# Performance work log

Measured on AMD Instinct MI355X. Metric: run time of the kernel, lower is better.

Reference implementation:

```python
import jax, jax.numpy as jnp
import numpy as np

L, N, M = 128, 512, 256   # batch-like dim, recurrence length, feature dim (M_size1)
TK, H = 4, 8              # num_blocks, num_heads
DH = M // H
EPS = 1e-5


def setup_inputs() -> dict:
    key = jax.random.key(0)
    ks = jax.random.split(key, 8)
    s = 0.05  # scale raw-randn params for numerical stability
    return {
        "x": jax.random.normal(ks[0], (L, N, M), jnp.float32),
        "weight": jax.random.normal(ks[1], (M, M), jnp.float32) * s,
        "Wqkv": jax.random.normal(ks[2], (TK, 3, H, DH, M), jnp.float32) * s,
        "Wo": jax.random.normal(ks[3], (TK, M, M), jnp.float32) * s,
        "ln_g": jnp.ones((M,), jnp.float32),
        "ln_b": jnp.zeros((M,), jnp.float32),
        "lnz_g": jnp.ones((M,), jnp.float32),
        "lnz_b": jnp.zeros((M,), jnp.float32),
        "fc1_w": jax.random.normal(ks[4], (4 * M, M), jnp.float32) / np.float32(np.sqrt(M)),
        "fc1_b": jnp.zeros((4 * M,), jnp.float32),
        "fc2_w": jax.random.normal(ks[5], (M, 4 * M), jnp.float32) / np.float32(np.sqrt(4 * M)),
        "fc2_b": jnp.zeros((M,), jnp.float32),
    }


def _ln(x, g, b):
    mu = x.mean(-1, keepdims=True)
    var = x.var(-1, keepdims=True)  # biased variance, as torch LayerNorm
    return (x - mu) * jax.lax.rsqrt(var + EPS) * g + b


def _pos_bias(dtype):
    # bias[j, z]   = sin(j / 10000**(2z/M)) for even z
    # bias[j, z+1] = cos(j / 10000**(2z/M))
    pos = jnp.arange(N, dtype=dtype)                      # j
    z = jnp.arange(0, M, 2, dtype=dtype)                  # even indices
    ang = pos[:, None] / (10000.0 ** (2.0 * z / M))       # (N, M/2)
    return jnp.stack([jnp.sin(ang), jnp.cos(ang)], axis=-1).reshape(N, M)


def reference(x, weight, Wqkv, Wo, ln_g, ln_b, lnz_g, lnz_b, fc1_w, fc1_b, fc2_w, fc2_b):
    # savespace: (L, N, M); positional bias depends only on (j, feature)
    s = jnp.einsum('lm,ijm->ijl', weight, x) + _pos_bias(x.dtype)[None]
    inv_sqrt_dh = np.float32(1.0 / np.sqrt(DH))
    for a in range(TK):
        qkv = jnp.einsum('xhdm,ijm->xijhd', Wqkv[a], _ln(s, ln_g, ln_b))
        q, k, v = qkv[0], qkv[1], qkv[2]                  # each (L, N, H, DH)
        rsa = jnp.einsum('ijhd,ijhd->ijh', q * inv_sqrt_dh, k)
        imv = rsa[..., None] * v                           # (L, N, H, DH)
        imv = jnp.cumsum(imv, axis=1)                      # retention recurrence over j
        s = jnp.einsum('nm,ijm->ijn', Wo[a], imv.reshape(L, N, M)) + s
        s = _ln(s, lnz_g, lnz_b) + s
        h = jax.nn.gelu(s @ fc1_w.T + fc1_b, approximate=False)
        s = h @ fc2_w.T + fc2_b
    return s
```

## Files before the change

### kernel.cpp

```cpp
#include <hip/hip_runtime.h>

typedef unsigned int u32;
typedef unsigned short u16;
typedef _Float16 f16;
typedef __attribute__((ext_vector_type(8))) _Float16 f16x8;
typedef __attribute__((ext_vector_type(4))) float f32x4;
typedef __attribute__((ext_vector_type(4))) u16 u16x4;

#define L_ 128
#define N_ 512
#define M_ 256
#define TK_ 4
#define H_ 8
#define R_ (L_*N_)
#define FF_ 1024

__device__ __forceinline__ u16 f2h(float v){ f16 h=(f16)v; return __builtin_bit_cast(u16,h); }
__device__ __forceinline__ float h2f(u16 b){ return (float)__builtin_bit_cast(f16,b); }
__device__ __forceinline__ f32x4 mfmah(f16x8 a, f16x8 b, f32x4 c){
  return __builtin_amdgcn_mfma_f32_16x16x32_f16(a,b,c,0,0,0);
}
__device__ __forceinline__ float gelu_f(float x){
  float u = x*(0.7978845608f + 0.0356774081f*x*x);
  float e = __expf(u + u);
  float r = __builtin_amdgcn_rcpf(e + 1.f);
  return x - x*r;
}


__global__ void k_bias(float* __restrict__ bias){
  int j = blockIdx.x, l = threadIdx.x;
  int t = l>>1;
  float base = expf(-0.14391156831212757f * (float)t);
  float ang = (float)j * base;
  bias[j*M_ + l] = (l&1) ? cosf(ang) : sinf(ang);
}

__global__ void k_pack(const float* __restrict__ src, u16* __restrict__ dst, int K){
  int b = blockIdx.x; int nk = K>>6; int cg = b/nk, k64 = b%nk;
  int t = threadIdx.x;
  int st = t>>6, g = (t>>4)&3, lr = t&15;
  const float* sp = src + (cg*16+lr)*K + k64*64 + st*32 + g*8;
  f16x8 hv;
  #pragma unroll
  for (int e=0;e<8;e++) hv[e] = (f16)sp[e];
  *(f16x8*)(dst + b*1024 + t*8) = hv;
}

__global__ void k_pack_qkv(const float* __restrict__ w, u16* __restrict__ dst){
  int b = blockIdx.x;
  int a = b/192; int rmn = b%192; int grp = rmn>>2, k64 = rmn&3;
  int hd = grp/6, cidx = grp%6;
  int t = threadIdx.x;
  int st = t>>6, g = (t>>4)&3, lr = t&15;
  int cl = cidx*16 + lr;
  int x = cl>>5, d = cl&31;
  const float* sp = w + (((a*3+x)*H_+hd)*32 + d)*M_ + k64*64 + st*32 + g*8;
  f16x8 hv;
  #pragma unroll
  for (int e=0;e<8;e++) hv[e] = (f16)sp[e];
  *(f16x8*)(dst + b*1024 + t*8) = hv;
}

__device__ __forceinline__ void stageA16(const u16* __restrict__ src, u16* __restrict__ Abuf,
                                         int rowbase, int tid){
  int row = tid>>3, skh = tid&7;
  int k64 = skh>>1, st = skh&1;
  int rg = row>>4, lr = row&15;
  const u16* sp = src + (rowbase+row)*M_ + k64*64 + st*32;
  u16* dp = Abuf + (k64*4+rg)*1024 + st*512 + lr*8;
  #pragma unroll
  for (int gg=0;gg<4;gg++)
    *(uint4*)(dp + gg*128) = *(const uint4*)(sp + gg*8);
}

__global__ __launch_bounds__(512) void k_init(const float* __restrict__ X, const u16* __restrict__ Wf,
    const float* __restrict__ bias, const float* __restrict__ lg, const float* __restrict__ lb,
    float* __restrict__ out, u16* __restrict__ P1){
  __shared__ __align__(16) u16 Abuf[16*1024];
  __shared__ float zs[8][64][2];
  int tid = threadIdx.x;
  int wx = tid>>6, lane = tid&63;
  int g = lane>>4, lr = lane&15;
  int lo = g*128 + lr*8;
  int rowbase = blockIdx.x*64;
  {
    int row = tid>>3, skh = tid&7;
    int k64 = skh>>1, st = skh&1;
    int rg = row>>4, slr = row&15;
    const float* sp = X + (rowbase+row)*M_ + k64*64 + st*32;
    u16* dp = Abuf + (k64*4+rg)*1024 + st*512 + slr*8;
    #pragma unroll
    for (int gg=0;gg<4;gg++){
      f16x8 hv;
      #pragma unroll
      for (int e=0;e<8;e++) hv[e] = (f16)sp[gg*8+e];
      *(f16x8*)(dp + gg*128) = hv;
    }
  }
  __syncthreads();
  f32x4 acc[4][2];
  #pragma unroll
  for (int i=0;i<4;i++){ acc[i][0]=0.f; acc[i][1]=0.f; }
  #pragma unroll
  for (int k64=0;k64<4;k64++)
    #pragma unroll
    for (int st=0;st<2;st++){
      f16x8 a[4], b[2];
      #pragma unroll
      for (int i=0;i<4;i++) a[i] = *(const f16x8*)(Abuf + (k64*4 + i)*1024 + st*512 + lo);
      #pragma unroll
      for (int j=0;j<2;j++) b[j] = *(const f16x8*)(Wf + ((wx*2+j)*4 + k64)*1024 + st*512 + lo);
      #pragma unroll
      for (int i=0;i<4;i++)
        #pragma unroll
        for (int j=0;j<2;j++) acc[i][j] = mfmah(a[i], b[j], acc[i][j]);
    }
  #pragma unroll
  for (int i=0;i<4;i++)
    #pragma unroll
    for (int j=0;j<2;j++)
      #pragma unroll
      for (int r=0;r<4;r++){
        int row = rowbase + i*16 + g*4 + r;
        int col = wx*32 + j*16 + lr;
        acc[i][j][r] += bias[(row & (N_-1))*M_ + col];
        out[row*M_ + col] = acc[i][j][r];
      }
  #pragma unroll
  for (int i=0;i<4;i++)
    #pragma unroll
    for (int r=0;r<4;r++){
      float ps = 0.f, qs = 0.f;
      #pragma unroll
      for (int j=0;j<2;j++){ float t = acc[i][j][r]; ps += t; qs += t*t; }
      ps += __shfl_xor(ps,1); qs += __shfl_xor(qs,1);
      ps += __shfl_xor(ps,2); qs += __shfl_xor(qs,2);
      ps += __shfl_xor(ps,4); qs += __shfl_xor(qs,4);
      ps += __shfl_xor(ps,8); qs += __shfl_xor(qs,8);
      if (lr == 0){
        int rowl = i*16 + g*4 + r;
        zs[wx][rowl][0] = ps;
        zs[wx][rowl][1] = qs;
      }
    }
  __syncthreads();
  #pragma unroll
  for (int i=0;i<4;i++)
    #pragma unroll
    for (int r=0;r<4;r++){
      int rowl = i*16 + g*4 + r;
      float sum=0.f, sq=0.f;
      #pragma unroll
      for (int q=0;q<8;q++){ sum += zs[q][rowl][0]; sq += zs[q][rowl][1]; }
      float mean = sum*(1.f/M_);
      float var  = sq*(1.f/M_) - mean*mean;
      float rstd = rsqrtf(var + 1e-5f);
      int row = rowbase + rowl;
      #pragma unroll
      for (int j=0;j<2;j++){
        int col = wx*32 + j*16 + lr;
        P1[row*M_ + col] = f2h((acc[i][j][r]-mean)*rstd*lg[col] + lb[col]);
      }
    }
}

__global__ __launch_bounds__(512) void k_qkv(const u16* __restrict__ P1, const u16* __restrict__ Wq,
    u16* __restrict__ imv){
  __shared__ __align__(16) u16 Abuf[16*1024];
  int tid = threadIdx.x;
  int hd = tid>>6, lane = tid&63;
  int g = lane>>4, lr = lane&15;
  int lo = g*128 + lr*8;
  int rowbase = blockIdx.x*64;
  stageA16(P1, Abuf, rowbase, tid);
  __syncthreads();
  f32x4 acc[4][6];
  #pragma unroll
  for (int i=0;i<4;i++)
    #pragma unroll
    for (int c=0;c<6;c++) acc[i][c] = 0.f;
  const u16* Wb = Wq + hd*6*4096;
  #pragma unroll
  for (int k64=0;k64<4;k64++)
    #pragma unroll
    for (int st=0;st<2;st++){
      f16x8 a[4];
      #pragma unroll
      for (int i=0;i<4;i++) a[i] = *(const f16x8*)(Abuf + (k64*4 + i)*1024 + st*512 + lo);
      #pragma unroll
      for (int c=0;c<6;c++){
        f16x8 b = *(const f16x8*)(Wb + (c*4 + k64)*1024 + st*512 + lo);
        #pragma unroll
        for (int i=0;i<4;i++) acc[i][c] = mfmah(a[i], b, acc[i][c]);
      }
    }
  const float isd = 0.17677669529663687f;
  #pragma unroll
  for (int i=0;i<4;i++){
    f32x4 p = acc[i][0]*acc[i][2] + acc[i][1]*acc[i][3];
    #pragma unroll
    for (int r=0;r<4;r++){
      float v = p[r];
      v += __shfl_xor(v,1); v += __shfl_xor(v,2);
      v += __shfl_xor(v,4); v += __shfl_xor(v,8);
      float rsa = v * isd;
      int row = rowbase + i*16 + g*4 + r;
      imv[row*M_ + hd*32 + lr]      = f2h(rsa*acc[i][4][r]);
      imv[row*M_ + hd*32 + 16 + lr] = f2h(rsa*acc[i][5][r]);
    }
  }
}

__global__ __launch_bounds__(256) void k_scan(const u16* __restrict__ imv, u16* __restrict__ P1){
  __shared__ float tot[4][64];
  int bi = blockIdx.x;
  int i = bi>>2, mc = bi&3;
  int tid = threadIdx.x;
  int ml = tid&63, jc = tid>>6;
  int m = mc*64 + ml;
  int base = i*N_*M_ + jc*128*M_ + m;
  float acc = 0.f;
  for (int jb=0;jb<128;jb+=8){
    float t[8];
    #pragma unroll
    for (int u=0;u<8;u++) t[u] = h2f(imv[base + (jb+u)*M_]);
    #pragma unroll
    for (int u=0;u<8;u++) acc += t[u];
  }
  tot[jc][ml] = acc;
  __syncthreads();
  float pre = 0.f;
  #pragma unroll
  for (int q=0;q<3;q++) if (q<jc) pre += tot[q][ml];
  acc = pre;
  for (int jb=0;jb<128;jb+=8){
    float t[8];
    #pragma unroll
    for (int u=0;u<8;u++) t[u] = h2f(imv[base + (jb+u)*M_]);
    #pragma unroll
    for (int u=0;u<8;u++){ acc += t[u]; P1[base + (jb+u)*M_] = f2h(acc); }
  }
}

__global__ __launch_bounds__(512) void k_wo(u16* __restrict__ P1, const u16* __restrict__ Wf,
    const float* __restrict__ sold, const float* __restrict__ lg, const float* __restrict__ lb){
  __shared__ __align__(16) u16 Abuf[16*1024];
  __shared__ float zs[8][64][2];
  int tid = threadIdx.x;
  int wx = tid>>6, lane = tid&63;
  int g = lane>>4, lr = lane&15;
  int lo = g*128 + lr*8;
  int rowbase = blockIdx.x*64;
  stageA16(P1, Abuf, rowbase, tid);
  __syncthreads();
  f32x4 acc[4][2];
  #pragma unroll
  for (int i=0;i<4;i++){ acc[i][0]=0.f; acc[i][1]=0.f; }
  #pragma unroll
  for (int k64=0;k64<4;k64++)
    #pragma unroll
    for (int st=0;st<2;st++){
      f16x8 a[4], b[2];
      #pragma unroll
      for (int i=0;i<4;i++) a[i] = *(const f16x8*)(Abuf + (k64*4 + i)*1024 + st*512 + lo);
      #pragma unroll
      for (int j=0;j<2;j++) b[j] = *(const f16x8*)(Wf + ((wx*2+j)*4 + k64)*1024 + st*512 + lo);
      #pragma unroll
      for (int i=0;i<4;i++)
        #pragma unroll
        for (int j=0;j<2;j++) acc[i][j] = mfmah(a[i], b[j], acc[i][j]);
    }
  #pragma unroll
  for (int i=0;i<4;i++)
    #pragma unroll
    for (int j=0;j<2;j++)
      #pragma unroll
      for (int r=0;r<4;r++){
        int row = rowbase + i*16 + g*4 + r;
        int col = wx*32 + j*16 + lr;
        acc[i][j][r] += sold[row*M_ + col];
      }
  #pragma unroll
  for (int i=0;i<4;i++)
    #pragma unroll
    for (int r=0;r<4;r++){
      float ps = 0.f, qs = 0.f;
      #pragma unroll
      for (int j=0;j<2;j++){ float t = acc[i][j][r]; ps += t; qs += t*t; }
      ps += __shfl_xor(ps,1); qs += __shfl_xor(qs,1);
      ps += __shfl_xor(ps,2); qs += __shfl_xor(qs,2);
      ps += __shfl_xor(ps,4); qs += __shfl_xor(qs,4);
      ps += __shfl_xor(ps,8); qs += __shfl_xor(qs,8);
      if (lr == 0){
        int rowl = i*16 + g*4 + r;
        zs[wx][rowl][0] = ps;
        zs[wx][rowl][1] = qs;
      }
    }
  __syncthreads();
  #pragma unroll
  for (int i=0;i<4;i++)
    #pragma unroll
    for (int r=0;r<4;r++){
      int rowl = i*16 + g*4 + r;
      float sum=0.f, sq=0.f;
      #pragma unroll
      for (int q=0;q<8;q++){ sum += zs[q][rowl][0]; sq += zs[q][rowl][1]; }
      float mean = sum*(1.f/M_);
      float var  = sq*(1.f/M_) - mean*mean;
      float rstd = rsqrtf(var + 1e-5f);
      int row = rowbase + rowl;
      #pragma unroll
      for (int j=0;j<2;j++){
        int col = wx*32 + j*16 + lr;
        float zv = acc[i][j][r];
        P1[row*M_ + col] = f2h((zv-mean)*rstd*lg[col] + lb[col] + zv);
      }
    }
}

__global__ __launch_bounds__(512) void k_fc(u16* __restrict__ P1,
    const u16* __restrict__ W1f, const float* __restrict__ b1,
    const u16* __restrict__ W2f, const float* __restrict__ b2,
    const float* __restrict__ lg, const float* __restrict__ lb,
    float* __restrict__ out){
  __shared__ __align__(16) u16 Abuf[16*1024];
  __shared__ __align__(16) u16 Hbuf[64*128];
  __shared__ float zs[8][64][2];
  int tid = threadIdx.x;
  int wx = tid>>6, lane = tid&63;
  int g = lane>>4, lr = lane&15;
  int lo = g*128 + lr*8;
  int rowbase = blockIdx.x*64;
  stageA16(P1, Abuf, rowbase, tid);
  __syncthreads();
  f32x4 acc2[4][2];
  #pragma unroll
  for (int i=0;i<4;i++){ acc2[i][0]=0.f; acc2[i][1]=0.f; }
  for (int c=0;c<8;c++){
    f32x4 acc1[4];
    #pragma unroll
    for (int j=0;j<4;j++) acc1[j] = 0.f;
    #pragma unroll
    for (int k64=0;k64<4;k64++)
      #pragma unroll
      for (int st=0;st<2;st++){
        f16x8 aw = *(const f16x8*)(W1f + ((c*8 + wx)*4 + k64)*1024 + st*512 + lo);
        #pragma unroll
        for (int j=0;j<4;j++){
          f16x8 bs = *(const f16x8*)(Abuf + (k64*4 + j)*1024 + st*512 + lo);
          acc1[j] = mfmah(aw, bs, acc1[j]);
        }
      }
    __syncthreads();
    {
      int fl = wx*16 + g*4;
      int kc = fl>>6, kloc = fl&63;
      float4 b1v = *(const float4*)(b1 + c*128 + fl);
      float bb[4] = {b1v.x, b1v.y, b1v.z, b1v.w};
      #pragma unroll
      for (int j=0;j<4;j++){
        int row = j*16 + lr;
        u16x4 hv;
        #pragma unroll
        for (int r=0;r<4;r++){
          float xv = acc1[j][r] + bb[r];
          hv[r] = f2h(gelu_f(xv));
        }
        int phys = ((kloc>>3) ^ row) & 7;
        *(u16x4*)(Hbuf + row*128 + kc*64 + phys*8 + (kloc&7)) = hv;
      }
    }
    __syncthreads();
    #pragma unroll
    for (int kcl=0;kcl<2;kcl++)
      #pragma unroll
      for (int st=0;st<2;st++){
        f16x8 ah[4], bb2[2];
        #pragma unroll
        for (int j=0;j<2;j++)
          bb2[j] = *(const f16x8*)(W2f + ((wx*2+j)*16 + c*2 + kcl)*1024 + st*512 + lo);
        #pragma unroll
        for (int i=0;i<4;i++){
          int hrow = i*16 + lr;
          int phys = (((st<<2)|g) ^ hrow) & 7;
          ah[i] = *(const f16x8*)(Hbuf + hrow*128 + kcl*64 + phys*8);
        }
        #pragma unroll
        for (int i=0;i<4;i++)
          #pragma unroll
          for (int j=0;j<2;j++) acc2[i][j] = mfmah(ah[i], bb2[j], acc2[i][j]);
      }
  }
  #pragma unroll
  for (int i=0;i<4;i++)
    #pragma unroll
    for (int j=0;j<2;j++)
      #pragma unroll
      for (int r=0;r<4;r++){
        int row = rowbase + i*16 + g*4 + r;
        int col = wx*32 + j*16 + lr;
        acc2[i][j][r] += b2[col];
        out[row*M_ + col] = acc2[i][j][r];
      }
  #pragma unroll
  for (int i=0;i<4;i++)
    #pragma unroll
    for (int r=0;r<4;r++){
      float ps = 0.f, qs = 0.f;
      #pragma unroll
      for (int j=0;j<2;j++){ float t = acc2[i][j][r]; ps += t; qs += t*t; }
      ps += __shfl_xor(ps,1); qs += __shfl_xor(qs,1);
      ps += __shfl_xor(ps,2); qs += __shfl_xor(qs,2);
      ps += __shfl_xor(ps,4); qs += __shfl_xor(qs,4);
      ps += __shfl_xor(ps,8); qs += __shfl_xor(qs,8);
      if (lr == 0){
        int rowl = i*16 + g*4 + r;
        zs[wx][rowl][0] = ps;
        zs[wx][rowl][1] = qs;
      }
    }
  __syncthreads();
  #pragma unroll
  for (int i=0;i<4;i++)
    #pragma unroll
    for (int r=0;r<4;r++){
      int rowl = i*16 + g*4 + r;
      float sum=0.f, sq=0.f;
      #pragma unroll
      for (int q=0;q<8;q++){ sum += zs[q][rowl][0]; sq += zs[q][rowl][1]; }
      float mean = sum*(1.f/M_);
      float var  = sq*(1.f/M_) - mean*mean;
      float rstd = rsqrtf(var + 1e-5f);
      int row = rowbase + rowl;
      #pragma unroll
      for (int j=0;j<2;j++){
        int col = wx*32 + j*16 + lr;
        P1[row*M_ + col] = f2h((acc2[i][j][r]-mean)*rstd*lg[col] + lb[col]);
      }
    }
}

extern "C" void kernel_launch(void* const* d_in, const int* in_sizes, int n_in,
                              void* d_out, int out_size, void* d_ws, size_t ws_size,
                              hipStream_t stream){
  const float* x      = (const float*)d_in[0];
  const float* weight = (const float*)d_in[1];
  const float* wqkv   = (const float*)d_in[2];
  const float* wo     = (const float*)d_in[3];
  const float* ln_g   = (const float*)d_in[4];
  const float* ln_b   = (const float*)d_in[5];
  const float* lnz_g  = (const float*)d_in[6];
  const float* lnz_b  = (const float*)d_in[7];
  const float* fc1_w  = (const float*)d_in[8];
  const float* fc1_b  = (const float*)d_in[9];
  const float* fc2_w  = (const float*)d_in[10];
  const float* fc2_b  = (const float*)d_in[11];
  float* out = (float*)d_out;
  char* ws = (char*)d_ws;
  size_t off = 0;
  u16* wqkvf = (u16*)(ws + off); off += 1572864;
  u16* wof   = (u16*)(ws + off); off += 524288;
  u16* fc1f  = (u16*)(ws + off); off += 524288;
  u16* fc2f  = (u16*)(ws + off); off += 524288;
  u16* P1    = (u16*)(ws + off); off += 33554432;
  u16* imv   = (u16*)(ws + off); off += 33554432;
  float* bias   = (float*)imv;
  u16*   weightf = (u16*)((char*)imv + 524288);

  k_bias<<<N_, M_, 0, stream>>>(bias);
  k_pack<<<64, 128, 0, stream>>>(weight, weightf, 256);
  k_pack_qkv<<<768, 128, 0, stream>>>(wqkv, wqkvf);
  k_pack<<<256, 128, 0, stream>>>(wo, wof, 256);
  k_pack<<<256, 128, 0, stream>>>(fc1_w, fc1f, 256);
  k_pack<<<256, 128, 0, stream>>>(fc2_w, fc2f, 1024);
  k_init<<<R_/64, 512, 0, stream>>>(x, weightf, bias, ln_g, ln_b, out, P1);
  for (int a=0; a<TK_; a++){
    k_qkv<<<R_/64, 512, 0, stream>>>(P1, wqkvf + a*196608, imv);
    k_scan<<<L_*4, 256, 0, stream>>>(imv, P1);
    k_wo<<<R_/64, 512, 0, stream>>>(P1, wof + a*65536, out, lnz_g, lnz_b);
    k_fc<<<R_/64, 512, 0, stream>>>(P1, fc1f, fc1_b, fc2f, fc2_b, ln_g, ln_b, out);
  }
}
```

Baseline: 860.7 us.

## Fuse init/Wo/FC kernels with next block's QKV projection via shared-memory staging

Merges k_init with the first QKV projection, and k_wo, k_fc and the next block's QKV into one kernel. The normalized activations are written straight into the shared-memory A tile instead of round-tripping P1 through global memory, which removes several launches and fp16 global reads and writes per block. The QKV phase is split into a QK pass followed by a V pass to lower register pressure. Launch bounds now request 4 blocks per SM. The FC1 loop also hoists its weight loads. The risks are higher register and LDS pressure in the larger fused kernel, which could cut occupancy or cause spills.

Result: slower. 1.056 ms (+22.7%).

```diff
diff --git a/kernel.cpp b/kernel.cpp
--- a/kernel.cpp
+++ b/kernel.cpp
@@ -74,9 +74,77 @@
     *(uint4*)(dp + gg*128) = *(const uint4*)(sp + gg*8);
 }
 
-__global__ __launch_bounds__(512) void k_init(const float* __restrict__ X, const u16* __restrict__ Wf,
-    const float* __restrict__ bias, const float* __restrict__ lg, const float* __restrict__ lb,
-    float* __restrict__ out, u16* __restrict__ P1){
+__device__ __forceinline__ void val_to_abuf(u16* __restrict__ Abuf, float v,
+    int wx, int g, int lr, int i, int j, int r){
+  Abuf[((wx>>1)*4 + i)*1024 + (wx&1)*512 + (j*2+(lr>>3))*128 + (g*4+r)*8 + (lr&7)] = f2h(v);
+}
+
+__device__ __forceinline__ void qkv_phase(const u16* __restrict__ Abuf, const u16* __restrict__ Wq,
+    u16* __restrict__ imv, int rowbase, int hd, int g, int lr, int lo){
+  const u16* Wb = Wq + hd*6*4096;
+  const float isd = 0.17677669529663687f;
+  f32x4 aqk[4][4];
+  #pragma unroll
+  for (int i=0;i<4;i++)
+    #pragma unroll
+    for (int c=0;c<4;c++) aqk[i][c] = 0.f;
+  #pragma unroll
+  for (int k64=0;k64<4;k64++)
+    #pragma unroll
+    for (int st=0;st<2;st++){
+      f16x8 a[4];
+      #pragma unroll
+      for (int i=0;i<4;i++) a[i] = *(const f16x8*)(Abuf + (k64*4 + i)*1024 + st*512 + lo);
+      #pragma unroll
+      for (int c=0;c<4;c++){
+        f16x8 b = *(const f16x8*)(Wb + (c*4 + k64)*1024 + st*512 + lo);
+        #pragma unroll
+        for (int i=0;i<4;i++) aqk[i][c] = mfmah(a[i], b, aqk[i][c]);
+      }
+    }
+  float rsa[4][4];
+  #pragma unroll
+  for (int i=0;i<4;i++){
+    f32x4 p = aqk[i][0]*aqk[i][2] + aqk[i][1]*aqk[i][3];
+    #pragma unroll
+    for (int r=0;r<4;r++){
+      float v = p[r];
+      v += __shfl_xor(v,1); v += __shfl_xor(v,2);
+      v += __shfl_xor(v,4); v += __shfl_xor(v,8);
+      rsa[i][r] = v * isd;
+    }
+  }
+  f32x4 av[4][2];
+  #pragma unroll
+  for (int i=0;i<4;i++){ av[i][0]=0.f; av[i][1]=0.f; }
+  #pragma unroll
+  for (int k64=0;k64<4;k64++)
+    #pragma unroll
+    for (int st=0;st<2;st++){
+      f16x8 a[4];
+      #pragma unroll
+      for (int i=0;i<4;i++) a[i] = *(const f16x8*)(Abuf + (k64*4 + i)*1024 + st*512 + lo);
+      #pragma unroll
+      for (int c=0;c<2;c++){
+        f16x8 b = *(const f16x8*)(Wb + ((4+c)*4 + k64)*1024 + st*512 + lo);
+        #pragma unroll
+        for (int i=0;i<4;i++) av[i][c] = mfmah(a[i], b, av[i][c]);
+      }
+    }
+  #pragma unroll
+  for (int i=0;i<4;i++)
+    #pragma unroll
+    for (int r=0;r<4;r++){
+      int row = rowbase + i*16 + g*4 + r;
+      imv[row*M_ + hd*32 + lr]      = f2h(rsa[i][r]*av[i][0][r]);
+      imv[row*M_ + hd*32 + 16 + lr] = f2h(rsa[i][r]*av[i][1][r]);
+    }
+}
+
+__global__ __launch_bounds__(512,4) void k_initqkv(const float* __restrict__ X,
+    const u16* __restrict__ Wf, const float* __restrict__ bias,
+    const float* __restrict__ lg, const float* __restrict__ lb,
+    const u16* __restrict__ Wq, float* __restrict__ out, u16* __restrict__ imv){
   __shared__ __align__(16) u16 Abuf[16*1024];
   __shared__ float zs[8][64][2];
   int tid = threadIdx.x;
@@ -156,60 +224,14 @@
       float mean = sum*(1.f/M_);
       float var  = sq*(1.f/M_) - mean*mean;
       float rstd = rsqrtf(var + 1e-5f);
-      int row = rowbase + rowl;
       #pragma unroll
       for (int j=0;j<2;j++){
         int col = wx*32 + j*16 + lr;
-        P1[row*M_ + col] = f2h((acc[i][j][r]-mean)*rstd*lg[col] + lb[col]);
-      }
-    }
-}
-
-__global__ __launch_bounds__(512) void k_qkv(const u16* __restrict__ P1, const u16* __restrict__ Wq,
-    u16* __restrict__ imv){
-  __shared__ __align__(16) u16 Abuf[16*1024];
-  int tid = threadIdx.x;
-  int hd = tid>>6, lane = tid&63;
-  int g = lane>>4, lr = lane&15;
-  int lo = g*128 + lr*8;
-  int rowbase = blockIdx.x*64;
-  stageA16(P1, Abuf, rowbase, tid);
-  __syncthreads();
-  f32x4 acc[4][6];
-  #pragma unroll
-  for (int i=0;i<4;i++)
-    #pragma unroll
-    for (int c=0;c<6;c++) acc[i][c] = 0.f;
-  const u16* Wb = Wq + hd*6*4096;
-  #pragma unroll
-  for (int k64=0;k64<4;k64++)
-    #pragma unroll
-    for (int st=0;st<2;st++){
-      f16x8 a[4];
-      #pragma unroll
-      for (int i=0;i<4;i++) a[i] = *(const f16x8*)(Abuf + (k64*4 + i)*1024 + st*512 + lo);
-      #pragma unroll
-      for (int c=0;c<6;c++){
-        f16x8 b = *(const f16x8*)(Wb + (c*4 + k64)*1024 + st*512 + lo);
-        #pragma unroll
-        for (int i=0;i<4;i++) acc[i][c] = mfmah(a[i], b, acc[i][c]);
-      }
-    }
-  const float isd = 0.17677669529663687f;
-  #pragma unroll
-  for (int i=0;i<4;i++){
-    f32x4 p = acc[i][0]*acc[i][2] + acc[i][1]*acc[i][3];
-    #pragma unroll
-    for (int r=0;r<4;r++){
-      float v = p[r];
-      v += __shfl_xor(v,1); v += __shfl_xor(v,2);
-      v += __shfl_xor(v,4); v += __shfl_xor(v,8);
-      float rsa = v * isd;
-      int row = rowbase + i*16 + g*4 + r;
-      imv[row*M_ + hd*32 + lr]      = f2h(rsa*acc[i][4][r]);
-      imv[row*M_ + hd*32 + 16 + lr] = f2h(rsa*acc[i][5][r]);
-    }
-  }
+        val_to_abuf(Abuf, (acc[i][j][r]-mean)*rstd*lg[col] + lb[col], wx,g,lr,i,j,r);
+      }
+    }
+  __syncthreads();
+  qkv_phase(Abuf, Wq, imv, rowbase, wx, g, lr, lo);
 }
 
 __global__ __launch_bounds__(256) void k_scan(const u16* __restrict__ imv, u16* __restrict__ P1){
@@ -243,9 +265,16 @@
   }
 }
 
-__global__ __launch_bounds__(512) void k_wo(u16* __restrict__ P1, const u16* __restrict__ Wf,
-    const float* __restrict__ sold, const float* __restrict__ lg, const float* __restrict__ lb){
+template<int QKV>
+__global__ __launch_bounds__(512,4) void k_wofcqkv(const u16* __restrict__ P1,
+    const u16* __restrict__ Wof,
+    const u16* __restrict__ W1f, const float* __restrict__ b1,
+    const u16* __restrict__ W2f, const float* __restrict__ b2,
+    const float* __restrict__ lgz, const float* __restrict__ lbz,
+    const float* __restrict__ lg, const float* __restrict__ lb,
+    const u16* __restrict__ Wq, float* __restrict__ out, u16* __restrict__ imv){
   __shared__ __align__(16) u16 Abuf[16*1024];
+  __shared__ __align__(16) u16 Hbuf[64*128];
   __shared__ float zs[8][64][2];
   int tid = threadIdx.x;
   int wx = tid>>6, lane = tid&63;
@@ -265,7 +294,7 @@
       #pragma unroll
       for (int i=0;i<4;i++) a[i] = *(const f16x8*)(Abuf + (k64*4 + i)*1024 + st*512 + lo);
       #pragma unroll
-      for (int j=0;j<2;j++) b[j] = *(const f16x8*)(Wf + ((wx*2+j)*4 + k64)*1024 + st*512 + lo);
+      for (int j=0;j<2;j++) b[j] = *(const f16x8*)(Wof + ((wx*2+j)*4 + k64)*1024 + st*512 + lo);
       #pragma unroll
       for (int i=0;i<4;i++)
         #pragma unroll
@@ -279,7 +308,7 @@
       for (int r=0;r<4;r++){
         int row = rowbase + i*16 + g*4 + r;
         int col = wx*32 + j*16 + lr;
-        acc[i][j][r] += sold[row*M_ + col];
+        acc[i][j][r] += out[row*M_ + col];
       }
   #pragma unroll
   for (int i=0;i<4;i++)
@@ -310,30 +339,13 @@
       float mean = sum*(1.f/M_);
       float var  = sq*(1.f/M_) - mean*mean;
       float rstd = rsqrtf(var + 1e-5f);
-      int row = rowbase + rowl;
       #pragma unroll
       for (int j=0;j<2;j++){
         int col = wx*32 + j*16 + lr;
         float zv = acc[i][j][r];
-        P1[row*M_ + col] = f2h((zv-mean)*rstd*lg[col] + lb[col] + zv);
-      }
-    }
-}
-
-__global__ __launch_bounds__(512) void k_fc(u16* __restrict__ P1,
-    const u16* __restrict__ W1f, const float* __restrict__ b1,
-    const u16* __restrict__ W2f, const float* __restrict__ b2,
-    const float* __restrict__ lg, const float* __restrict__ lb,
-    float* __restrict__ out){
-  __shared__ __align__(16) u16 Abuf[16*1024];
-  __shared__ __align__(16) u16 Hbuf[64*128];
-  __shared__ float zs[8][64][2];
-  int tid = threadIdx.x;
-  int wx = tid>>6, lane = tid&63;
-  int g = lane>>4, lr = lane&15;
-  int lo = g*128 + lr*8;
-  int rowbase = blockIdx.x*64;
-  stageA16(P1, Abuf, rowbase, tid);
+        val_to_abuf(Abuf, (zv-mean)*rstd*lgz[col] + lbz[col] + zv, wx,g,lr,i,j,r);
+      }
+    }
   __syncthreads();
   f32x4 acc2[4][2];
   #pragma unroll
@@ -343,16 +355,21 @@
     #pragma unroll
     for (int j=0;j<4;j++) acc1[j] = 0.f;
     #pragma unroll
-    for (int k64=0;k64<4;k64++)
-      #pragma unroll
-      for (int st=0;st<2;st++){
-        f16x8 aw = *(const f16x8*)(W1f + ((c*8 + wx)*4 + k64)*1024 + st*512 + lo);
-        #pragma unroll
-        for (int j=0;j<4;j++){
-          f16x8 bs = *(const f16x8*)(Abuf + (k64*4 + j)*1024 + st*512 + lo);
-          acc1[j] = mfmah(aw, bs, acc1[j]);
-        }
-      }
+    for (int h=0;h<2;h++){
+      f16x8 aw[4];
+      #pragma unroll
+      for (int q=0;q<4;q++)
+        aw[q] = *(const f16x8*)(W1f + ((c*8 + wx)*4 + h*2 + (q>>1))*1024 + (q&1)*512 + lo);
+      #pragma unroll
+      for (int k2=0;k2<2;k2++)
+        #pragma unroll
+        for (int st=0;st<2;st++)
+          #pragma unroll
+          for (int j=0;j<4;j++){
+            f16x8 bs = *(const f16x8*)(Abuf + ((h*2+k2)*4 + j)*1024 + st*512 + lo);
+            acc1[j] = mfmah(aw[k2*2+st], bs, acc1[j]);
+          }
+    }
     __syncthreads();
     {
       int fl = wx*16 + g*4;
@@ -364,10 +381,8 @@
         int row = j*16 + lr;
         u16x4 hv;
         #pragma unroll
-        for (int r=0;r<4;r++){
-          float xv = acc1[j][r] + bb[r];
-          hv[r] = f2h(gelu_f(xv));
-        }
+        for (int r=0;r<4;r++)
+          hv[r] = f2h(gelu_f(acc1[j][r] + bb[r]));
         int phys = ((kloc>>3) ^ row) & 7;
         *(u16x4*)(Hbuf + row*128 + kc*64 + phys*8 + (kloc&7)) = hv;
       }
@@ -404,42 +419,45 @@
         acc2[i][j][r] += b2[col];
         out[row*M_ + col] = acc2[i][j][r];
       }
-  #pragma unroll
-  for (int i=0;i<4;i++)
-    #pragma unroll
-    for (int r=0;r<4;r++){
-      float ps = 0.f, qs = 0.f;
-      #pragma unroll
-      for (int j=0;j<2;j++){ float t = acc2[i][j][r]; ps += t; qs += t*t; }
-      ps += __shfl_xor(ps,1); qs += __shfl_xor(qs,1);
-      ps += __shfl_xor(ps,2); qs += __shfl_xor(qs,2);
-      ps += __shfl_xor(ps,4); qs += __shfl_xor(qs,4);
-      ps += __shfl_xor(ps,8); qs += __shfl_xor(qs,8);
-      if (lr == 0){
+  if (QKV){
+    #pragma unroll
+    for (int i=0;i<4;i++)
+      #pragma unroll
+      for (int r=0;r<4;r++){
+        float ps = 0.f, qs = 0.f;
+        #pragma unroll
+        for (int j=0;j<2;j++){ float t = acc2[i][j][r]; ps += t; qs += t*t; }
+        ps += __shfl_xor(ps,1); qs += __shfl_xor(qs,1);
+        ps += __shfl_xor(ps,2); qs += __shfl_xor(qs,2);
+        ps += __shfl_xor(ps,4); qs += __shfl_xor(qs,4);
+        ps += __shfl_xor(ps,8); qs += __shfl_xor(qs,8);
+        if (lr == 0){
+          int rowl = i*16 + g*4 + r;
+          zs[wx][rowl][0] = ps;
+          zs[wx][rowl][1] = qs;
+        }
+      }
+    __syncthreads();
+    #pragma unroll
+    for (int i=0;i<4;i++)
+      #pragma unroll
+      for (int r=0;r<4;r++){
         int rowl = i*16 + g*4 + r;
-        zs[wx][rowl][0] = ps;
-        zs[wx][rowl][1] = qs;
-      }
-    }
-  __syncthreads();
-  #pragma unroll
-  for (int i=0;i<4;i++)
-    #pragma unroll
-    for (int r=0;r<4;r++){
-      int rowl = i*16 + g*4 + r;
-      float sum=0.f, sq=0.f;
-      #pragma unroll
-      for (int q=0;q<8;q++){ sum += zs[q][rowl][0]; sq += zs[q][rowl][1]; }
-      float mean = sum*(1.f/M_);
-      float var  = sq*(1.f/M_) - mean*mean;
-      float rstd = rsqrtf(var + 1e-5f);
-      int row = rowbase + rowl;
-      #pragma unroll
-      for (int j=0;j<2;j++){
-        int col = wx*32 + j*16 + lr;
-        P1[row*M_ + col] = f2h((acc2[i][j][r]-mean)*rstd*lg[col] + lb[col]);
-      }
-    }
+        float sum=0.f, sq=0.f;
+        #pragma unroll
+        for (int q=0;q<8;q++){ sum += zs[q][rowl][0]; sq += zs[q][rowl][1]; }
+        float mean = sum*(1.f/M_);
+        float var  = sq*(1.f/M_) - mean*mean;
+        float rstd = rsqrtf(var + 1e-5f);
+        #pragma unroll
+        for (int j=0;j<2;j++){
+          int col = wx*32 + j*16 + lr;
+          val_to_abuf(Abuf, (acc2[i][j][r]-mean)*rstd*lg[col] + lb[col], wx,g,lr,i,j,r);
+        }
+      }
+    __syncthreads();
+    qkv_phase(Abuf, Wq, imv, rowbase, wx, g, lr, lo);
+  }
 }
 
 extern "C" void kernel_launch(void* const* d_in, const int* in_sizes, int n_in,
@@ -460,14 +478,14 @@
   float* out = (float*)d_out;
   char* ws = (char*)d_ws;
   size_t off = 0;
-  u16* wqkvf = (u16*)(ws + off); off += 1572864;
-  u16* wof   = (u16*)(ws + off); off += 524288;
-  u16* fc1f  = (u16*)(ws + off); off += 524288;
-  u16* fc2f  = (u16*)(ws + off); off += 524288;
-  u16* P1    = (u16*)(ws + off); off += 33554432;
-  u16* imv   = (u16*)(ws + off); off += 33554432;
-  float* bias   = (float*)imv;
-  u16*   weightf = (u16*)((char*)imv + 524288);
+  u16* wqkvf   = (u16*)(ws + off); off += 1572864;
+  u16* wof     = (u16*)(ws + off); off += 524288;
+  u16* fc1f    = (u16*)(ws + off); off += 524288;
+  u16* fc2f    = (u16*)(ws + off); off += 524288;
+  u16* weightf = (u16*)(ws + off); off += 131072;
+  float* bias  = (float*)(ws + off); off += 524288;
+  u16* P1      = (u16*)(ws + off); off += 33554432;
+  u16* imv     = (u16*)(ws + off); off += 33554432;
 
   k_bias<<<N_, M_, 0, stream>>>(bias);
   k_pack<<<64, 128, 0, stream>>>(weight, weightf, 256);
@@ -475,11 +493,14 @@
   k_pack<<<256, 128, 0, stream>>>(wo, wof, 256);
   k_pack<<<256, 128, 0, stream>>>(fc1_w, fc1f, 256);
   k_pack<<<256, 128, 0, stream>>>(fc2_w, fc2f, 1024);
-  k_init<<<R_/64, 512, 0, stream>>>(x, weightf, bias, ln_g, ln_b, out, P1);
+  k_initqkv<<<R_/64, 512, 0, stream>>>(x, weightf, bias, ln_g, ln_b, wqkvf, out, imv);
   for (int a=0; a<TK_; a++){
-    k_qkv<<<R_/64, 512, 0, stream>>>(P1, wqkvf + a*196608, imv);
     k_scan<<<L_*4, 256, 0, stream>>>(imv, P1);
-    k_wo<<<R_/64, 512, 0, stream>>>(P1, wof + a*65536, out, lnz_g, lnz_b);
-    k_fc<<<R_/64, 512, 0, stream>>>(P1, fc1f, fc1_b, fc2f, fc2_b, ln_g, ln_b, out);
-  }
-}
+    if (a < TK_-1)
+      k_wofcqkv<1><<<R_/64, 512, 0, stream>>>(P1, wof + a*65536, fc1f, fc1_b, fc2f, fc2_b,
+          lnz_g, lnz_b, ln_g, ln_b, wqkvf + (a+1)*196608, out, imv);
+    else
+      k_wofcqkv<0><<<R_/64, 512, 0, stream>>>(P1, wof + a*65536, fc1f, fc1_b, fc2f, fc2_b,
+          lnz_g, lnz_b, ln_g, ln_b, (const u16*)nullptr, out, (u16*)nullptr);
+  }
+}
```

## Fuse Wo projection, LayerNorm residual and FC MLP into one kernel

Applied to the files above, without the earlier changes.

Merges k_wo and k_fc into a single kernel that keeps the post-LayerNorm activations in shared memory (written directly into the MFMA A-buffer layout) instead of round-tripping them through P1 in global memory. The hidden buffer is double-buffered across FC chunks so one barrier per chunk can be dropped, and fc1 weight loads are batched per half. It also moves weightf and bias out of the imv scratch region. It removes one kernel launch and a 32MB write plus read per block, at the cost of higher shared-memory use per workgroup, which may lower occupancy.

Result: slower. 1.010 ms (+17.4%).

```diff
diff --git a/kernel.cpp b/kernel.cpp
--- a/kernel.cpp
+++ b/kernel.cpp
@@ -72,6 +72,11 @@
   #pragma unroll
   for (int gg=0;gg<4;gg++)
     *(uint4*)(dp + gg*128) = *(const uint4*)(sp + gg*8);
+}
+
+__device__ __forceinline__ void val_to_abuf(u16* __restrict__ Abuf, float v,
+    int wx, int g, int lr, int i, int j, int r){
+  Abuf[((wx>>1)*4 + i)*1024 + (wx&1)*512 + (j*2+(lr>>3))*128 + (g*4+r)*8 + (lr&7)] = f2h(v);
 }
 
 __global__ __launch_bounds__(512) void k_init(const float* __restrict__ X, const u16* __restrict__ Wf,
@@ -243,9 +248,14 @@
   }
 }
 
-__global__ __launch_bounds__(512) void k_wo(u16* __restrict__ P1, const u16* __restrict__ Wf,
-    const float* __restrict__ sold, const float* __restrict__ lg, const float* __restrict__ lb){
+__global__ __launch_bounds__(512) void k_wofc(u16* __restrict__ P1, const u16* __restrict__ Wof,
+    const u16* __restrict__ W1f, const float* __restrict__ b1,
+    const u16* __restrict__ W2f, const float* __restrict__ b2,
+    const float* __restrict__ lgz, const float* __restrict__ lbz,
+    const float* __restrict__ lg, const float* __restrict__ lb,
+    float* __restrict__ out){
   __shared__ __align__(16) u16 Abuf[16*1024];
+  __shared__ __align__(16) u16 Hbuf[2][64*128];
   __shared__ float zs[8][64][2];
   int tid = threadIdx.x;
   int wx = tid>>6, lane = tid&63;
@@ -265,7 +275,7 @@
       #pragma unroll
       for (int i=0;i<4;i++) a[i] = *(const f16x8*)(Abuf + (k64*4 + i)*1024 + st*512 + lo);
       #pragma unroll
-      for (int j=0;j<2;j++) b[j] = *(const f16x8*)(Wf + ((wx*2+j)*4 + k64)*1024 + st*512 + lo);
+      for (int j=0;j<2;j++) b[j] = *(const f16x8*)(Wof + ((wx*2+j)*4 + k64)*1024 + st*512 + lo);
       #pragma unroll
       for (int i=0;i<4;i++)
         #pragma unroll
@@ -279,7 +289,7 @@
       for (int r=0;r<4;r++){
         int row = rowbase + i*16 + g*4 + r;
         int col = wx*32 + j*16 + lr;
-        acc[i][j][r] += sold[row*M_ + col];
+        acc[i][j][r] += out[row*M_ + col];
       }
   #pragma unroll
   for (int i=0;i<4;i++)
@@ -310,50 +320,38 @@
       float mean = sum*(1.f/M_);
       float var  = sq*(1.f/M_) - mean*mean;
       float rstd = rsqrtf(var + 1e-5f);
-      int row = rowbase + rowl;
       #pragma unroll
       for (int j=0;j<2;j++){
         int col = wx*32 + j*16 + lr;
         float zv = acc[i][j][r];
-        P1[row*M_ + col] = f2h((zv-mean)*rstd*lg[col] + lb[col] + zv);
-      }
-    }
-}
-
-__global__ __launch_bounds__(512) void k_fc(u16* __restrict__ P1,
-    const u16* __restrict__ W1f, const float* __restrict__ b1,
-    const u16* __restrict__ W2f, const float* __restrict__ b2,
-    const float* __restrict__ lg, const float* __restrict__ lb,
-    float* __restrict__ out){
-  __shared__ __align__(16) u16 Abuf[16*1024];
-  __shared__ __align__(16) u16 Hbuf[64*128];
-  __shared__ float zs[8][64][2];
-  int tid = threadIdx.x;
-  int wx = tid>>6, lane = tid&63;
-  int g = lane>>4, lr = lane&15;
-  int lo = g*128 + lr*8;
-  int rowbase = blockIdx.x*64;
-  stageA16(P1, Abuf, rowbase, tid);
+        val_to_abuf(Abuf, (zv-mean)*rstd*lgz[col] + lbz[col] + zv, wx,g,lr,i,j,r);
+      }
+    }
   __syncthreads();
   f32x4 acc2[4][2];
   #pragma unroll
   for (int i=0;i<4;i++){ acc2[i][0]=0.f; acc2[i][1]=0.f; }
   for (int c=0;c<8;c++){
+    u16* Hb = Hbuf[c&1];
     f32x4 acc1[4];
     #pragma unroll
     for (int j=0;j<4;j++) acc1[j] = 0.f;
     #pragma unroll
-    for (int k64=0;k64<4;k64++)
-      #pragma unroll
-      for (int st=0;st<2;st++){
-        f16x8 aw = *(const f16x8*)(W1f + ((c*8 + wx)*4 + k64)*1024 + st*512 + lo);
-        #pragma unroll
-        for (int j=0;j<4;j++){
-          f16x8 bs = *(const f16x8*)(Abuf + (k64*4 + j)*1024 + st*512 + lo);
-          acc1[j] = mfmah(aw, bs, acc1[j]);
-        }
-      }
-    __syncthreads();
+    for (int h=0;h<2;h++){
+      f16x8 aw[4];
+      #pragma unroll
+      for (int q=0;q<4;q++)
+        aw[q] = *(const f16x8*)(W1f + ((c*8 + wx)*4 + h*2 + (q>>1))*1024 + (q&1)*512 + lo);
+      #pragma unroll
+      for (int k2=0;k2<2;k2++)
+        #pragma unroll
+        for (int st=0;st<2;st++)
+          #pragma unroll
+          for (int j=0;j<4;j++){
+            f16x8 bs = *(const f16x8*)(Abuf + ((h*2+k2)*4 + j)*1024 + st*512 + lo);
+            acc1[j] = mfmah(aw[k2*2+st], bs, acc1[j]);
+          }
+    }
     {
       int fl = wx*16 + g*4;
       int kc = fl>>6, kloc = fl&63;
@@ -364,12 +362,10 @@
         int row = j*16 + lr;
         u16x4 hv;
         #pragma unroll
-        for (int r=0;r<4;r++){
-          float xv = acc1[j][r] + bb[r];
-          hv[r] = f2h(gelu_f(xv));
-        }
+        for (int r=0;r<4;r++)
+          hv[r] = f2h(gelu_f(acc1[j][r] + bb[r]));
         int phys = ((kloc>>3) ^ row) & 7;
-        *(u16x4*)(Hbuf + row*128 + kc*64 + phys*8 + (kloc&7)) = hv;
+        *(u16x4*)(Hb + row*128 + kc*64 + phys*8 + (kloc&7)) = hv;
       }
     }
     __syncthreads();
@@ -385,7 +381,7 @@
         for (int i=0;i<4;i++){
           int hrow = i*16 + lr;
           int phys = (((st<<2)|g) ^ hrow) & 7;
-          ah[i] = *(const f16x8*)(Hbuf + hrow*128 + kcl*64 + phys*8);
+          ah[i] = *(const f16x8*)(Hb + hrow*128 + kcl*64 + phys*8);
         }
         #pragma unroll
         for (int i=0;i<4;i++)
@@ -460,14 +456,14 @@
   float* out = (float*)d_out;
   char* ws = (char*)d_ws;
   size_t off = 0;
-  u16* wqkvf = (u16*)(ws + off); off += 1572864;
-  u16* wof   = (u16*)(ws + off); off += 524288;
-  u16* fc1f  = (u16*)(ws + off); off += 524288;
-  u16* fc2f  = (u16*)(ws + off); off += 524288;
-  u16* P1    = (u16*)(ws + off); off += 33554432;
-  u16* imv   = (u16*)(ws + off); off += 33554432;
-  float* bias   = (float*)imv;
-  u16*   weightf = (u16*)((char*)imv + 524288);
+  u16* wqkvf   = (u16*)(ws + off); off += 1572864;
+  u16* wof     = (u16*)(ws + off); off += 524288;
+  u16* fc1f    = (u16*)(ws + off); off += 524288;
+  u16* fc2f    = (u16*)(ws + off); off += 524288;
+  u16* weightf = (u16*)(ws + off); off += 131072;
+  float* bias  = (float*)(ws + off); off += 524288;
+  u16* P1      = (u16*)(ws + off); off += 33554432;
+  u16* imv     = (u16*)(ws + off); off += 33554432;
 
   k_bias<<<N_, M_, 0, stream>>>(bias);
   k_pack<<<64, 128, 0, stream>>>(weight, weightf, 256);
@@ -479,7 +475,7 @@
   for (int a=0; a<TK_; a++){
     k_qkv<<<R_/64, 512, 0, stream>>>(P1, wqkvf + a*196608, imv);
     k_scan<<<L_*4, 256, 0, stream>>>(imv, P1);
-    k_wo<<<R_/64, 512, 0, stream>>>(P1, wof + a*65536, out, lnz_g, lnz_b);
-    k_fc<<<R_/64, 512, 0, stream>>>(P1, fc1f, fc1_b, fc2f, fc2_b, ln_g, ln_b, out);
-  }
-}
+    k_wofc<<<R_/64, 512, 0, stream>>>(P1, wof + a*65536, fc1f, fc1_b, fc2f, fc2_b,
+        lnz_g, lnz_b, ln_g, ln_b, out);
+  }
+}
```
